# Optimization experiments

Measured on AMD Instinct MI355X. Metric: run time of the kernel, lower is better.

The kernel has to match this reference:

```python
import jax, jax.numpy as jnp
import numpy as np

B, C, H, W = 16, 384, 56, 56
NH, WS, SS = 12, 7, 3          # num_heads, window_size, shift_size
MLP = 4 * C
N = WS * WS                     # tokens per window (49)
nHW = H // WS                   # windows per side (8)
nW = nHW * nHW                  # windows per image (64)
HD = C // NH                    # head dim (32)
EPS = 1e-5


def _ln(x, g, b):
    mu = jnp.mean(x, axis=-1, keepdims=True)
    var = jnp.mean(jnp.square(x - mu), axis=-1, keepdims=True)
    return (x - mu) * jax.lax.rsqrt(var + EPS) * g + b


def _attn_mask():
    # static shifted-window mask, computed once with numpy (constants)
    img = np.zeros((H, W))
    sl = (slice(0, -WS), slice(-WS, -SS), slice(-SS, None))
    cnt = 0
    for hs in sl:
        for ws_ in sl:
            img[hs, ws_] = cnt
            cnt += 1
    mw = img.reshape(nHW, WS, nHW, WS).transpose(0, 2, 1, 3).reshape(-1, N)
    d = mw[:, None, :] - mw[:, :, None]          # (nW, N, N)
    return jnp.asarray(np.where(d != 0, -100.0, 0.0), jnp.float32)

_MASK = _attn_mask()


def setup_inputs() -> dict:
    key = jax.random.key(0)
    ks = jax.random.split(key, 6)
    rn = lambda k, s: jax.random.normal(k, s, jnp.float32) * 0.02
    return {
        "x": jax.random.normal(ks[0], (B, C, H, W), jnp.float32),
        "norm1_g": jnp.ones((C,), jnp.float32),
        "norm1_b": jnp.zeros((C,), jnp.float32),
        "qkv_w": rn(ks[1], (C, 3 * C)),
        "qkv_b": jnp.zeros((3 * C,), jnp.float32),
        "proj_w": rn(ks[2], (C, C)),
        "proj_b": jnp.zeros((C,), jnp.float32),
        "norm2_g": jnp.ones((C,), jnp.float32),
        "norm2_b": jnp.zeros((C,), jnp.float32),
        "fc1_w": rn(ks[3], (C, MLP)),
        "fc1_b": jnp.zeros((MLP,), jnp.float32),
        "fc2_w": rn(ks[4], (MLP, C)),
        "fc2_b": jnp.zeros((C,), jnp.float32),
    }


def reference(x, norm1_g, norm1_b, qkv_w, qkv_b, proj_w, proj_b,
              norm2_g, norm2_b, fc1_w, fc1_b, fc2_w, fc2_b):
    shortcut = x                                   # (B, C, H, W)
    xh = jnp.transpose(x, (0, 2, 3, 1))            # (B, H, W, C)
    xh = _ln(xh, norm1_g, norm1_b)
    # H, W divisible by WS -> padding is a no-op; shifted window path
    xs = jnp.roll(xh, (-SS, -SS), axis=(1, 2))
    # window partition -> (B*nW, N, C)
    xw = xs.reshape(B, nHW, WS, nHW, WS, C).transpose(0, 1, 3, 2, 4, 5)
    xw = xw.reshape(-1, N, C)
    # attention
    qkv = (xw @ qkv_w + qkv_b).reshape(-1, N, 3, NH, HD).transpose(2, 0, 3, 1, 4)
    q, k, v = qkv[0] * HD ** -0.5, qkv[1], qkv[2]  # (B*nW, NH, N, HD)
    attn = jnp.einsum('whnd,whmd->whnm', q, k)     # (B*nW, NH, N, N)
    attn = attn.reshape(B, nW, NH, N, N) + _MASK[None, :, None]
    attn = jax.nn.softmax(attn, axis=-1).reshape(-1, NH, N, N)
    out = jnp.einsum('whnm,whmd->whnd', attn, v)   # (B*nW, NH, N, HD)
    out = out.transpose(0, 2, 1, 3).reshape(-1, N, C)
    out = out @ proj_w + proj_b
    # window reverse -> (B, H, W, C), un-shift
    xs = out.reshape(B, nHW, nHW, WS, WS, C).transpose(0, 1, 3, 2, 4, 5)
    xs = xs.reshape(B, H, W, C)
    xh = jnp.roll(xs, (SS, SS), axis=(1, 2))
    x2 = shortcut + jnp.transpose(xh, (0, 3, 1, 2))
    # MLP residual (in BHWC)
    xh2 = jnp.transpose(x2, (0, 2, 3, 1))
    h = jax.nn.gelu(_ln(xh2, norm2_g, norm2_b) @ fc1_w + fc1_b,
                    approximate=False) @ fc2_w + fc2_b
    xh2 = xh2 + h
    return jnp.transpose(xh2, (0, 3, 1, 2))
```

## Files before the change

### kernel.cpp

```cpp
#include <hip/hip_runtime.h>
#include <hip/hip_bf16.h>
#include <math.h>
#include <stdint.h>

#define C_ 384
#define TOKENS 50176

typedef __bf16 bf16;
typedef __bf16 bf16x8 __attribute__((ext_vector_type(8)));
typedef __bf16 bf16x4 __attribute__((ext_vector_type(4)));
typedef float  f32x4  __attribute__((ext_vector_type(4)));

__device__ __forceinline__ float b2f(bf16 x) { return (float)x; }
__device__ __forceinline__ bf16  f2b(float x) { return (bf16)x; }

__device__ __forceinline__ float fast_gelu(float v) {
    float u2 = v * fmaf(v * v, 0.07135481f, 1.5957691f);
    return v / (1.0f + __expf(-u2));
}

__device__ __forceinline__ void gld_lds16(const bf16* g, bf16* l) {
    __builtin_amdgcn_global_load_lds(
        (const __attribute__((address_space(1))) void*)g,
        (__attribute__((address_space(3))) void*)l, 16, 0, 0);
}

__global__ void wtrans_kernel(const float* __restrict__ in, bf16* __restrict__ out,
                              int K, int N) {
    int idx = blockIdx.x * 256 + threadIdx.x;
    if (idx >= K * N) return;
    int n = idx / K, k = idx % K;
    out[idx] = f2b(in[(size_t)k * N + n]);
}

__global__ __launch_bounds__(256) void ln1_gather_kernel(
    const float* __restrict__ x, const float* __restrict__ g,
    const float* __restrict__ bt, bf16* __restrict__ xw) {
    int wave = threadIdx.x >> 6, lane = threadIdx.x & 63;
    int T = blockIdx.x * 4 + wave;
    int wi = T / 49, n = T % 49;
    int b = wi >> 6, w64 = wi & 63;
    int bh = w64 >> 3, bw = w64 & 7;
    int hs = bh * 7 + n / 7 + 3; if (hs >= 56) hs -= 56;
    int wsd = bw * 7 + n % 7 + 3; if (wsd >= 56) wsd -= 56;
    const float* xp = x + (size_t)b * C_ * 3136 + hs * 56 + wsd;
    float v[6];
    #pragma unroll
    for (int k = 0; k < 6; k++) v[k] = xp[(size_t)(lane + k * 64) * 3136];
    float s = v[0] + v[1] + v[2] + v[3] + v[4] + v[5];
    #pragma unroll
    for (int m = 32; m; m >>= 1) s += __shfl_xor(s, m);
    float mu = s * (1.0f / 384.0f);
    float s2 = 0.f;
    #pragma unroll
    for (int k = 0; k < 6; k++) { float d = v[k] - mu; s2 += d * d; }
    #pragma unroll
    for (int m = 32; m; m >>= 1) s2 += __shfl_xor(s2, m);
    float rstd = rsqrtf(s2 * (1.0f / 384.0f) + 1e-5f);
    bf16* op = xw + (size_t)T * 384;
    #pragma unroll
    for (int k = 0; k < 6; k++) {
        int c = lane + k * 64;
        op[c] = f2b((v[k] - mu) * rstd * g[c] + bt[c]);
    }
}

enum { EPI_NONE = 0, EPI_GELU = 1, EPI_PROJ = 2, EPI_FC2 = 3 };

__device__ __forceinline__ void stage_tile(const bf16* const (&gA)[4], bf16* const (&lA)[4],
                                           const bf16* const (&gB)[2], bf16* const (&lB)[2],
                                           int k0) {
    #pragma unroll
    for (int p = 0; p < 4; p++) gld_lds16(gA[p] + k0, lA[p]);
    #pragma unroll
    for (int p = 0; p < 2; p++) gld_lds16(gB[p] + k0, lB[p]);
}

__device__ __forceinline__ void compute_tile(const bf16* Asb, const bf16* Bsb,
                                             int wr, int wc, int quad, int lm,
                                             f32x4 (&acc)[4][4]) {
    #pragma unroll
    for (int kk = 0; kk < 2; kk++) {
        bf16x8 af[4], bfr[4];
        #pragma unroll
        for (int i = 0; i < 4; i++) {
            int row = wr * 64 + i * 16 + lm;
            int g = (kk * 4 + quad) ^ (row & 7);
            af[i] = *(const bf16x8*)(Asb + row * 64 + g * 8);
        }
        #pragma unroll
        for (int j = 0; j < 4; j++) {
            int row = wc * 64 + j * 16 + lm;
            int g = (kk * 4 + quad) ^ (row & 7);
            bfr[j] = *(const bf16x8*)(Bsb + row * 64 + g * 8);
        }
        __builtin_amdgcn_s_setprio(1);
        #pragma unroll
        for (int j = 0; j < 4; j++)
            #pragma unroll
            for (int i = 0; i < 4; i++)
                acc[j][i] = __builtin_amdgcn_mfma_f32_16x16x32_bf16(bfr[j], af[i], acc[j][i], 0, 0, 0);
        __builtin_amdgcn_s_setprio(0);
    }
}

#define SYNC_FENCE() do { __builtin_amdgcn_sched_barrier(0); \
                          __builtin_amdgcn_s_barrier(); \
                          __builtin_amdgcn_sched_barrier(0); } while (0)

template <int EPI>
__global__ __launch_bounds__(512, 2) void gemm_kernel(
    const bf16* __restrict__ A, const bf16* __restrict__ Wt,
    const float* __restrict__ bias, bf16* __restrict__ Cout,
    int Kdim, int Ndim,
    const float* __restrict__ resx,
    const bf16* __restrict__ resb) {
    __shared__ __align__(16) bf16 As[2][256 * 64];
    __shared__ __align__(16) bf16 Bs[2][128 * 64];
    int t = threadIdx.x;

    int nwg = gridDim.x * gridDim.y;
    int bid = blockIdx.y * gridDim.x + blockIdx.x;
    int q8 = nwg >> 3, r8 = nwg & 7, xcd = bid & 7, off = bid >> 3;
    int swz = (xcd < r8 ? xcd * (q8 + 1) : r8 * (q8 + 1) + (xcd - r8) * q8) + off;
    int n0 = (swz % gridDim.x) * 128;
    int m0 = (swz / gridDim.x) * 256;

    int lane = t & 63, wave = t >> 6;
    int wr = wave >> 1, wc = wave & 1;
    int quad = lane >> 4, lm = lane & 15;
    f32x4 acc[4][4] = {};

    const bf16* gA[4]; bf16* lA0[4]; bf16* lA1[4];
    const bf16* gB[2]; bf16* lB0[2]; bf16* lB1[2];
    #pragma unroll
    for (int p = 0; p < 4; p++) {
        int idx = p * 512 + t;
        int row = idx >> 3, g = idx & 7;
        int gs = g ^ (row & 7);
        gA[p] = A + (size_t)(m0 + row) * Kdim + gs * 8;
        lA0[p] = &As[0][idx * 8]; lA1[p] = &As[1][idx * 8];
    }
    #pragma unroll
    for (int p = 0; p < 2; p++) {
        int idx = p * 512 + t;
        int row = idx >> 3, g = idx & 7;
        int gs = g ^ (row & 7);
        gB[p] = Wt + (size_t)(n0 + row) * Kdim + gs * 8;
        lB0[p] = &Bs[0][idx * 8]; lB1[p] = &Bs[1][idx * 8];
    }

    int nt = Kdim >> 6;
    stage_tile(gA, lA0, gB, lB0, 0);
    stage_tile(gA, lA1, gB, lB1, 64);
    asm volatile("s_waitcnt vmcnt(6)" ::: "memory");
    SYNC_FENCE();

    for (int tk = 0; tk < nt; tk += 2) {
        compute_tile(As[0], Bs[0], wr, wc, quad, lm, acc);
        SYNC_FENCE();
        if (tk + 2 < nt) {
            stage_tile(gA, lA0, gB, lB0, (tk + 2) << 6);
            asm volatile("s_waitcnt vmcnt(6)" ::: "memory");
        } else {
            asm volatile("s_waitcnt vmcnt(0)" ::: "memory");
        }
        SYNC_FENCE();
        compute_tile(As[1], Bs[1], wr, wc, quad, lm, acc);
        if (tk + 2 < nt) {
            SYNC_FENCE();
            if (tk + 3 < nt) {
                stage_tile(gA, lA1, gB, lB1, (tk + 3) << 6);
                asm volatile("s_waitcnt vmcnt(6)" ::: "memory");
            } else {
                asm volatile("s_waitcnt vmcnt(0)" ::: "memory");
            }
            SYNC_FENCE();
        }
    }

    #pragma unroll
    for (int i = 0; i < 4; i++) {
        int m = m0 + wr * 64 + i * 16 + lm;
        size_t resbase = 0;
        if (EPI == EPI_PROJ) {
            int wi = m / 49, n_ = m % 49;
            int b = wi >> 6, w64 = wi & 63;
            int bh = w64 >> 3, bw = w64 & 7;
            int hs = bh * 7 + n_ / 7 + 3; if (hs >= 56) hs -= 56;
            int wsd = bw * 7 + n_ % 7 + 3; if (wsd >= 56) wsd -= 56;
            resbase = (size_t)b * C_ * 3136 + hs * 56 + wsd;
        }
        #pragma unroll
        for (int j = 0; j < 4; j++) {
            int nb = n0 + wc * 64 + j * 16 + quad * 4;
            f32x4 bj = *(const f32x4*)(bias + nb);
            f32x4 v;
            #pragma unroll
            for (int r = 0; r < 4; r++) v[r] = acc[j][i][r] + bj[r];
            if (EPI == EPI_GELU) {
                #pragma unroll
                for (int r = 0; r < 4; r++) v[r] = fast_gelu(v[r]);
            }
            if (EPI == EPI_PROJ) {
                #pragma unroll
                for (int r = 0; r < 4; r++) v[r] += resx[resbase + (size_t)(nb + r) * 3136];
            }
            if (EPI == EPI_FC2) {
                bf16x4 rb = *(const bf16x4*)(resb + (size_t)m * 384 + nb);
                #pragma unroll
                for (int r = 0; r < 4; r++) v[r] += b2f(rb[r]);
            }
            bf16x4 o;
            #pragma unroll
            for (int r = 0; r < 4; r++) o[r] = f2b(v[r]);
            *(bf16x4*)(Cout + (size_t)m * Ndim + nb) = o;
        }
    }
}

__global__ __launch_bounds__(64) void attn_mfma_kernel(const bf16* __restrict__ qkv,
                                                       bf16* __restrict__ aout) {
    __shared__ __align__(16) bf16 pbuf[64 * 72];
    __shared__ int reg_[64];
    int l = threadIdx.x;
    int wi = blockIdx.x / 12, h = blockIdx.x % 12;
    int i16 = l & 15, quad = l >> 4;

    {
        int tok = l < 49 ? l : 48;
        int w64 = wi & 63;
        int bh = w64 >> 3, bw = w64 & 7;
        int hh = bh * 7 + tok / 7, ww = bw * 7 + tok % 7;
        int fh = hh < 49 ? 0 : (hh < 53 ? 1 : 2);
        int fw = ww < 49 ? 0 : (ww < 53 ? 1 : 2);
        reg_[l] = fh * 3 + fw;
    }
    __syncthreads();

    const bf16* qbase = qkv + (size_t)wi * 49 * 1152 + h * 32;

    f32x4 s_[4][4] = {};
    bf16x8 af[4], bfr[4];
    #pragma unroll
    for (int mi = 0; mi < 4; mi++) {
        int m = mi * 16 + i16; if (m > 48) m = 48;
        af[mi] = *(const bf16x8*)(qbase + (size_t)m * 1152 + quad * 8);
    }
    #pragma unroll
    for (int nt = 0; nt < 4; nt++) {
        int n = nt * 16 + i16; if (n > 48) n = 48;
        bfr[nt] = *(const bf16x8*)(qbase + 384 + (size_t)n * 1152 + quad * 8);
    }
    #pragma unroll
    for (int mi = 0; mi < 4; mi++)
        #pragma unroll
        for (int nt = 0; nt < 4; nt++)
            s_[mi][nt] = __builtin_amdgcn_mfma_f32_16x16x32_bf16(af[mi], bfr[nt], s_[mi][nt], 0, 0, 0);

    int creg[4];
    #pragma unroll
    for (int nt = 0; nt < 4; nt++) {
        int c = nt * 16 + i16; if (c > 48) c = 48;
        creg[nt] = reg_[c];
    }

    const float scale = 0.17677669529663687f;
    #pragma unroll
    for (int mi = 0; mi < 4; mi++) {
        #pragma unroll
        for (int r = 0; r < 4; r++) {
            int row = mi * 16 + quad * 4 + r;
            int rreg = reg_[row];
            float v[4]; float mx = -1e30f;
            #pragma unroll
            for (int nt = 0; nt < 4; nt++) {
                int c = nt * 16 + i16;
                float x = s_[mi][nt][r] * scale;
                if (c > 48) x = -1e30f;
                else if (rreg != creg[nt]) x -= 100.0f;
                v[nt] = x; mx = fmaxf(mx, x);
            }
            #pragma unroll
            for (int m = 8; m; m >>= 1) mx = fmaxf(mx, __shfl_xor(mx, m));
            float sum = 0.f;
            #pragma unroll
            for (int nt = 0; nt < 4; nt++) { v[nt] = __expf(v[nt] - mx); sum += v[nt]; }
            #pragma unroll
            for (int m = 8; m; m >>= 1) sum += __shfl_xor(sum, m);
            float inv = 1.0f / sum;
            #pragma unroll
            for (int nt = 0; nt < 4; nt++)
                pbuf[row * 72 + nt * 16 + i16] = f2b(v[nt] * inv);
        }
    }
    __syncthreads();

    f32x4 o_[4][2] = {};
    const bf16* vbase = qkv + (size_t)wi * 49 * 1152 + 768 + h * 32;
    #pragma unroll
    for (int ks = 0; ks < 2; ks++) {
        bf16x8 pa[4];
        #pragma unroll
        for (int mi = 0; mi < 4; mi++)
            pa[mi] = *(const bf16x8*)(pbuf + (mi * 16 + i16) * 72 + ks * 32 + quad * 8);
        bf16x8 vb[2];
        #pragma unroll
        for (int nt = 0; nt < 2; nt++)
            #pragma unroll
            for (int j = 0; j < 8; j++) {
                int tok = ks * 32 + quad * 8 + j; if (tok > 48) tok = 48;
                vb[nt][j] = vbase[(size_t)tok * 1152 + nt * 16 + i16];
            }
        #pragma unroll
        for (int mi = 0; mi < 4; mi++)
            #pragma unroll
            for (int nt = 0; nt < 2; nt++)
                o_[mi][nt] = __builtin_amdgcn_mfma_f32_16x16x32_bf16(pa[mi], vb[nt], o_[mi][nt], 0, 0, 0);
    }

    bf16* obase = aout + (size_t)wi * 49 * 384 + h * 32;
    #pragma unroll
    for (int mi = 0; mi < 4; mi++)
        #pragma unroll
        for (int r = 0; r < 4; r++) {
            int row = mi * 16 + quad * 4 + r;
            if (row < 49) {
                #pragma unroll
                for (int nt = 0; nt < 2; nt++)
                    obase[(size_t)row * 384 + nt * 16 + i16] = f2b(o_[mi][nt][r]);
            }
        }
}

__global__ __launch_bounds__(256) void ln2_kernel(const bf16* __restrict__ x2,
                                                  const float* __restrict__ g,
                                                  const float* __restrict__ bt,
                                                  bf16* __restrict__ x2n) {
    int wave = threadIdx.x >> 6, lane = threadIdx.x & 63;
    int T = blockIdx.x * 4 + wave;
    const bf16* xp = x2 + (size_t)T * 384;
    float v[6];
    #pragma unroll
    for (int k = 0; k < 6; k++) v[k] = b2f(xp[lane + k * 64]);
    float s = v[0] + v[1] + v[2] + v[3] + v[4] + v[5];
    #pragma unroll
    for (int m = 32; m; m >>= 1) s += __shfl_xor(s, m);
    float mu = s * (1.0f / 384.0f);
    float s2 = 0.f;
    #pragma unroll
    for (int k = 0; k < 6; k++) { float d = v[k] - mu; s2 += d * d; }
    #pragma unroll
    for (int m = 32; m; m >>= 1) s2 += __shfl_xor(s2, m);
    float rstd = rsqrtf(s2 * (1.0f / 384.0f) + 1e-5f);
    bf16* op = x2n + (size_t)T * 384;
    #pragma unroll
    for (int k = 0; k < 6; k++) {
        int c = lane + k * 64;
        op[c] = f2b((v[k] - mu) * rstd * g[c] + bt[c]);
    }
}

__global__ __launch_bounds__(256) void untile_kernel(const bf16* __restrict__ otok,
                                                     float* __restrict__ out) {
    __shared__ float tile[56 * 65];
    int t = threadIdx.x;
    int b = blockIdx.x / 336;
    int rem = blockIdx.x % 336;
    int h = rem / 6;
    int c0 = (rem % 6) * 64;
    int hs = h + 53; if (hs >= 56) hs -= 56;
    int bh = hs / 7, th = hs % 7;
    #pragma unroll
    for (int pass = 0; pass < 14; pass++) {
        int w = pass * 4 + (t >> 6);
        int c = t & 63;
        int wsd = w + 53; if (wsd >= 56) wsd -= 56;
        int T = (b * 64 + bh * 8 + wsd / 7) * 49 + th * 7 + wsd % 7;
        tile[w * 65 + c] = b2f(otok[(size_t)T * 384 + c0 + c]);
    }
    __syncthreads();
    #pragma unroll
    for (int pass = 0; pass < 14; pass++) {
        int idx = pass * 256 + t;
        int c = idx / 56, w = idx % 56;
        out[((size_t)(b * 384 + c0 + c)) * 3136 + h * 56 + w] = tile[w * 65 + c];
    }
}

extern "C" void kernel_launch(void* const* d_in, const int* in_sizes, int n_in,
                              void* d_out, int out_size, void* d_ws, size_t ws_size,
                              hipStream_t stream) {
    (void)in_sizes; (void)n_in; (void)out_size; (void)ws_size;
    const float* x      = (const float*)d_in[0];
    const float* n1g    = (const float*)d_in[1];
    const float* n1b    = (const float*)d_in[2];
    const float* qkv_w  = (const float*)d_in[3];
    const float* qkv_b  = (const float*)d_in[4];
    const float* proj_w = (const float*)d_in[5];
    const float* proj_b = (const float*)d_in[6];
    const float* n2g    = (const float*)d_in[7];
    const float* n2b    = (const float*)d_in[8];
    const float* fc1_w  = (const float*)d_in[9];
    const float* fc1_b  = (const float*)d_in[10];
    const float* fc2_w  = (const float*)d_in[11];
    const float* fc2_b  = (const float*)d_in[12];
    float* out = (float*)d_out;
    char* ws = (char*)d_ws;

    bf16* qkv_wT = (bf16*)(ws + 0);
    bf16* proj_wT = (bf16*)(ws + 884736);
    bf16* fc1_wT = (bf16*)(ws + 1179648);
    bf16* fc2_wT = (bf16*)(ws + 2359296);
    bf16* xw   = (bf16*)(ws + 4194304);
    bf16* qkvb = (bf16*)(ws + 42729472);
    bf16* attn = (bf16*)(ws + 158334976);
    bf16* x2   = (bf16*)(ws + 4194304);
    bf16* x2n  = (bf16*)(ws + 42729472);
    bf16* h1   = (bf16*)(ws + 81264640);
    bf16* otok = (bf16*)(ws + 235405312);

    wtrans_kernel<<<(384 * 1152 + 255) / 256, 256, 0, stream>>>(qkv_w, qkv_wT, 384, 1152);
    wtrans_kernel<<<(384 * 384 + 255) / 256, 256, 0, stream>>>(proj_w, proj_wT, 384, 384);
    wtrans_kernel<<<(384 * 1536 + 255) / 256, 256, 0, stream>>>(fc1_w, fc1_wT, 384, 1536);
    wtrans_kernel<<<(1536 * 384 + 255) / 256, 256, 0, stream>>>(fc2_w, fc2_wT, 1536, 384);

    ln1_gather_kernel<<<TOKENS / 4, 256, 0, stream>>>(x, n1g, n1b, xw);

    gemm_kernel<EPI_NONE><<<dim3(9, 196), 512, 0, stream>>>(
        xw, qkv_wT, qkv_b, qkvb, 384, 1152, nullptr, nullptr);

    attn_mfma_kernel<<<12288, 64, 0, stream>>>(qkvb, attn);

    gemm_kernel<EPI_PROJ><<<dim3(3, 196), 512, 0, stream>>>(
        attn, proj_wT, proj_b, x2, 384, 384, x, nullptr);

    ln2_kernel<<<TOKENS / 4, 256, 0, stream>>>(x2, n2g, n2b, x2n);

    gemm_kernel<EPI_GELU><<<dim3(12, 196), 512, 0, stream>>>(
        x2n, fc1_wT, fc1_b, h1, 384, 1536, nullptr, nullptr);

    gemm_kernel<EPI_FC2><<<dim3(3, 196), 512, 0, stream>>>(
        h1, fc2_wT, fc2_b, otok, 1536, 384, nullptr, x2);

    untile_kernel<<<16 * 336, 256, 0, stream>>>(otok, out);
}
```

Measured before the change: 701.7 us.

## Shrink GEMM tile to 128x128 with 4 waves and batch LDS fragment loads

The GEMM block tile goes from 256x128 with 8 waves to 128x128 with 4 waves, and the grid doubles along M. The A and B staging now uses four 16-byte loads per thread each. The compute step loads both k-halves of the fragments up front using precomputed swizzled byte offsets, with sched barriers isolating the LDS reads from the MFMA chain. The aim is more blocks per CU, less LDS per block, and fewer address calculations in the inner loop. The cost is less operand reuse per block and more redundant weight reads.

```diff
diff --git a/kernel.cpp b/kernel.cpp
--- a/kernel.cpp
+++ b/kernel.cpp
@@ -67,41 +67,40 @@
 
 enum { EPI_NONE = 0, EPI_GELU = 1, EPI_PROJ = 2, EPI_FC2 = 3 };
 
-__device__ __forceinline__ void stage_tile(const bf16* const (&gA)[4], bf16* const (&lA)[4],
-                                           const bf16* const (&gB)[2], bf16* const (&lB)[2],
-                                           int k0) {
-    #pragma unroll
-    for (int p = 0; p < 4; p++) gld_lds16(gA[p] + k0, lA[p]);
-    #pragma unroll
-    for (int p = 0; p < 2; p++) gld_lds16(gB[p] + k0, lB[p]);
+__device__ __forceinline__ void stage_tile(const bf16* const (&gA)[4], const bf16* const (&gB)[4],
+                                           bf16* Asb, bf16* Bsb, int t, int k0) {
+    #pragma unroll
+    for (int p = 0; p < 4; p++) gld_lds16(gA[p] + k0, Asb + (p * 256 + t) * 8);
+    #pragma unroll
+    for (int p = 0; p < 4; p++) gld_lds16(gB[p] + k0, Bsb + (p * 256 + t) * 8);
 }
 
 __device__ __forceinline__ void compute_tile(const bf16* Asb, const bf16* Bsb,
-                                             int wr, int wc, int quad, int lm,
+                                             int aoff0, int aoff1, int boff0, int boff1,
                                              f32x4 (&acc)[4][4]) {
-    #pragma unroll
-    for (int kk = 0; kk < 2; kk++) {
-        bf16x8 af[4], bfr[4];
-        #pragma unroll
-        for (int i = 0; i < 4; i++) {
-            int row = wr * 64 + i * 16 + lm;
-            int g = (kk * 4 + quad) ^ (row & 7);
-            af[i] = *(const bf16x8*)(Asb + row * 64 + g * 8);
-        }
-        #pragma unroll
-        for (int j = 0; j < 4; j++) {
-            int row = wc * 64 + j * 16 + lm;
-            int g = (kk * 4 + quad) ^ (row & 7);
-            bfr[j] = *(const bf16x8*)(Bsb + row * 64 + g * 8);
-        }
-        __builtin_amdgcn_s_setprio(1);
+    bf16x8 af[2][4], bfr[2][4];
+    __builtin_amdgcn_sched_barrier(0);
+    #pragma unroll
+    for (int i = 0; i < 4; i++) {
+        af[0][i] = *(const bf16x8*)((const char*)Asb + aoff0 + i * 2048);
+        af[1][i] = *(const bf16x8*)((const char*)Asb + aoff1 + i * 2048);
+    }
+    #pragma unroll
+    for (int j = 0; j < 4; j++) {
+        bfr[0][j] = *(const bf16x8*)((const char*)Bsb + boff0 + j * 2048);
+        bfr[1][j] = *(const bf16x8*)((const char*)Bsb + boff1 + j * 2048);
+    }
+    __builtin_amdgcn_sched_barrier(0);
+    __builtin_amdgcn_s_setprio(1);
+    #pragma unroll
+    for (int kk = 0; kk < 2; kk++)
         #pragma unroll
         for (int j = 0; j < 4; j++)
             #pragma unroll
             for (int i = 0; i < 4; i++)
-                acc[j][i] = __builtin_amdgcn_mfma_f32_16x16x32_bf16(bfr[j], af[i], acc[j][i], 0, 0, 0);
-        __builtin_amdgcn_s_setprio(0);
-    }
+                acc[j][i] = __builtin_amdgcn_mfma_f32_16x16x32_bf16(bfr[kk][j], af[kk][i], acc[j][i], 0, 0, 0);
+    __builtin_amdgcn_s_setprio(0);
+    __builtin_amdgcn_sched_barrier(0);
 }
 
 #define SYNC_FENCE() do { __builtin_amdgcn_sched_barrier(0); \
@@ -109,13 +108,13 @@
                           __builtin_amdgcn_sched_barrier(0); } while (0)
 
 template <int EPI>
-__global__ __launch_bounds__(512, 2) void gemm_kernel(
+__global__ __launch_bounds__(256, 2) void gemm_kernel(
     const bf16* __restrict__ A, const bf16* __restrict__ Wt,
     const float* __restrict__ bias, bf16* __restrict__ Cout,
     int Kdim, int Ndim,
     const float* __restrict__ resx,
     const bf16* __restrict__ resb) {
-    __shared__ __align__(16) bf16 As[2][256 * 64];
+    __shared__ __align__(16) bf16 As[2][128 * 64];
     __shared__ __align__(16) bf16 Bs[2][128 * 64];
     int t = threadIdx.x;
 
@@ -124,54 +123,51 @@
     int q8 = nwg >> 3, r8 = nwg & 7, xcd = bid & 7, off = bid >> 3;
     int swz = (xcd < r8 ? xcd * (q8 + 1) : r8 * (q8 + 1) + (xcd - r8) * q8) + off;
     int n0 = (swz % gridDim.x) * 128;
-    int m0 = (swz / gridDim.x) * 256;
+    int m0 = (swz / gridDim.x) * 128;
 
     int lane = t & 63, wave = t >> 6;
     int wr = wave >> 1, wc = wave & 1;
     int quad = lane >> 4, lm = lane & 15;
     f32x4 acc[4][4] = {};
 
-    const bf16* gA[4]; bf16* lA0[4]; bf16* lA1[4];
-    const bf16* gB[2]; bf16* lB0[2]; bf16* lB1[2];
+    const bf16* gA[4]; const bf16* gB[4];
     #pragma unroll
     for (int p = 0; p < 4; p++) {
-        int idx = p * 512 + t;
+        int idx = p * 256 + t;
         int row = idx >> 3, g = idx & 7;
         int gs = g ^ (row & 7);
-        gA[p] = A + (size_t)(m0 + row) * Kdim + gs * 8;
-        lA0[p] = &As[0][idx * 8]; lA1[p] = &As[1][idx * 8];
-    }
-    #pragma unroll
-    for (int p = 0; p < 2; p++) {
-        int idx = p * 512 + t;
-        int row = idx >> 3, g = idx & 7;
-        int gs = g ^ (row & 7);
+        gA[p] = A  + (size_t)(m0 + row) * Kdim + gs * 8;
         gB[p] = Wt + (size_t)(n0 + row) * Kdim + gs * 8;
-        lB0[p] = &Bs[0][idx * 8]; lB1[p] = &Bs[1][idx * 8];
-    }
+    }
+
+    int g0 = quad ^ (lm & 7);
+    int aoff0 = ((wr * 64 + lm) * 64 + g0 * 8) * 2;
+    int boff0 = ((wc * 64 + lm) * 64 + g0 * 8) * 2;
+    int aoff1 = aoff0 ^ 64;
+    int boff1 = boff0 ^ 64;
 
     int nt = Kdim >> 6;
-    stage_tile(gA, lA0, gB, lB0, 0);
-    stage_tile(gA, lA1, gB, lB1, 64);
-    asm volatile("s_waitcnt vmcnt(6)" ::: "memory");
+    stage_tile(gA, gB, As[0], Bs[0], t, 0);
+    stage_tile(gA, gB, As[1], Bs[1], t, 64);
+    asm volatile("s_waitcnt vmcnt(8)" ::: "memory");
     SYNC_FENCE();
 
     for (int tk = 0; tk < nt; tk += 2) {
-        compute_tile(As[0], Bs[0], wr, wc, quad, lm, acc);
+        compute_tile(As[0], Bs[0], aoff0, aoff1, boff0, boff1, acc);
         SYNC_FENCE();
         if (tk + 2 < nt) {
-            stage_tile(gA, lA0, gB, lB0, (tk + 2) << 6);
-            asm volatile("s_waitcnt vmcnt(6)" ::: "memory");
+            stage_tile(gA, gB, As[0], Bs[0], t, (tk + 2) << 6);
+            asm volatile("s_waitcnt vmcnt(8)" ::: "memory");
         } else {
             asm volatile("s_waitcnt vmcnt(0)" ::: "memory");
         }
         SYNC_FENCE();
-        compute_tile(As[1], Bs[1], wr, wc, quad, lm, acc);
+        compute_tile(As[1], Bs[1], aoff0, aoff1, boff0, boff1, acc);
         if (tk + 2 < nt) {
             SYNC_FENCE();
             if (tk + 3 < nt) {
-                stage_tile(gA, lA1, gB, lB1, (tk + 3) << 6);
-                asm volatile("s_waitcnt vmcnt(6)" ::: "memory");
+                stage_tile(gA, gB, As[1], Bs[1], t, (tk + 3) << 6);
+                asm volatile("s_waitcnt vmcnt(8)" ::: "memory");
             } else {
                 asm volatile("s_waitcnt vmcnt(0)" ::: "memory");
             }
@@ -427,20 +423,20 @@
 
     ln1_gather_kernel<<<TOKENS / 4, 256, 0, stream>>>(x, n1g, n1b, xw);
 
-    gemm_kernel<EPI_NONE><<<dim3(9, 196), 512, 0, stream>>>(
+    gemm_kernel<EPI_NONE><<<dim3(9, 392), 256, 0, stream>>>(
         xw, qkv_wT, qkv_b, qkvb, 384, 1152, nullptr, nullptr);
 
     attn_mfma_kernel<<<12288, 64, 0, stream>>>(qkvb, attn);
 
-    gemm_kernel<EPI_PROJ><<<dim3(3, 196), 512, 0, stream>>>(
+    gemm_kernel<EPI_PROJ><<<dim3(3, 392), 256, 0, stream>>>(
         attn, proj_wT, proj_b, x2, 384, 384, x, nullptr);
 
     ln2_kernel<<<TOKENS / 4, 256, 0, stream>>>(x2, n2g, n2b, x2n);
 
-    gemm_kernel<EPI_GELU><<<dim3(12, 196), 512, 0, stream>>>(
+    gemm_kernel<EPI_GELU><<<dim3(12, 392), 256, 0, stream>>>(
         x2n, fc1_wT, fc1_b, h1, 384, 1536, nullptr, nullptr);
 
-    gemm_kernel<EPI_FC2><<<dim3(3, 196), 512, 0, stream>>>(
+    gemm_kernel<EPI_FC2><<<dim3(3, 392), 256, 0, stream>>>(
         h1, fc2_wT, fc2_b, otok, 1536, 384, nullptr, x2);
 
     untile_kernel<<<16 * 336, 256, 0, stream>>>(otok, out);
```

Result: faster. 654.0 us (-6.8%).
